# Kernel optimization log

Hardware: AMD Instinct MI355X
Metric: run time of the kernel (lower is better)

Reference implementation:

```python
import jax, jax.numpy as jnp
import numpy as np

ALPHA = 0.2  # LeakyReLU negative slope
NEG_INF = -9e15  # matches torch -9000000000000000.0


def setup_inputs() -> dict:
    key = jax.random.key(0)
    k1, k2, k3, k4, k5, k6 = jax.random.split(key, 6)
    N, F_in, F_out = 4096, 512, 256
    adj = jax.random.randint(k1, (N, N), 0, 2, dtype=jnp.int32)
    h = jax.random.normal(k2, (N, F_in), dtype=jnp.float32)
    # proj: Linear(F_in, F_out)
    W = jax.random.normal(k3, (F_in, F_out), dtype=jnp.float32) * (1.0 / np.sqrt(F_in))
    b = jax.random.normal(k4, (F_out,), dtype=jnp.float32) * 0.01
    # proj_a: Linear(2*F_out, 1) split into the two halves acting on src/dst features
    a1 = jax.random.normal(k5, (F_out,), dtype=jnp.float32) * (1.0 / np.sqrt(2 * F_out))
    a2 = jax.random.normal(k6, (F_out,), dtype=jnp.float32) * (1.0 / np.sqrt(2 * F_out))
    a_b = jnp.zeros((), dtype=jnp.float32)
    return {"adj": adj, "h": h, "W": W, "b": b, "a1": a1, "a2": a2, "a_b": a_b}


def reference(adj, h, W, b, a1, a2, a_b):
    # wh = proj(h): [N, F_out]
    wh = h @ W + b
    # Fused form of the N x N x 2F concat + Linear(2F,1):
    # logits[i, j] = wh[i] . a1 + wh[j] . a2 + a_b
    f_src = wh @ a1  # [N]
    f_dst = wh @ a2  # [N]
    e = jax.nn.leaky_relu(f_src[:, None] + f_dst[None, :] + a_b, negative_slope=ALPHA)
    e = jnp.where(adj > 0, e, NEG_INF)
    att = jax.nn.softmax(e, axis=-1)  # F.softmax legacy dim=1 for 2D
    # dropout: inference mode (no-op) for deterministic reference
    out = att @ wh  # [N, F_out]
    return jax.nn.elu(out)  # concat=True
```

## Files before the change

kernel.cpp:

```cpp
#include <hip/hip_runtime.h>

#define NN   4096
#define FIN  512
#define FOUT 256
#define ALPHA 0.2f

typedef __attribute__((ext_vector_type(8))) short short8;
typedef __attribute__((ext_vector_type(4))) float f32x4;
typedef unsigned short u16;

__device__ __forceinline__ u16 f2bf(float x) {
    union { float f; unsigned u; } v; v.f = x;
    unsigned r = v.u + 0x7FFF + ((v.u >> 16) & 1);
    return (u16)(r >> 16);
}

__global__ __launch_bounds__(256) void k_wt(const float* __restrict__ W,
                                            u16* __restrict__ Wt) {
    __shared__ float s[64 * 65];
    const int t  = threadIdx.x;
    const int f0 = blockIdx.x * 64;
    const int k0 = blockIdx.y * 64;
    #pragma unroll
    for (int p = 0; p < 4; ++p) {
        int q = t + 256 * p, rr = q >> 4, cc = q & 15;
        float4 w4 = *(const float4*)&W[(size_t)(k0 + rr) * FOUT + f0 + cc * 4];
        s[(cc * 4 + 0) * 65 + rr] = w4.x;
        s[(cc * 4 + 1) * 65 + rr] = w4.y;
        s[(cc * 4 + 2) * 65 + rr] = w4.z;
        s[(cc * 4 + 3) * 65 + rr] = w4.w;
    }
    __syncthreads();
    #pragma unroll
    for (int p = 0; p < 4; ++p) {
        int q = t + 256 * p, f = q >> 4, kg = q & 15;
        ushort4 o;
        o.x = f2bf(s[f * 65 + kg * 4 + 0]);
        o.y = f2bf(s[f * 65 + kg * 4 + 1]);
        o.z = f2bf(s[f * 65 + kg * 4 + 2]);
        o.w = f2bf(s[f * 65 + kg * 4 + 3]);
        *(ushort4*)&Wt[(size_t)(f0 + f) * FIN + k0 + kg * 4] = o;
    }
}

#define HS 520
__global__ __launch_bounds__(256) void k_proj(const float* __restrict__ h,
                                              const u16* __restrict__ Wt,
                                              const float* __restrict__ bias,
                                              const float* __restrict__ a1,
                                              const float* __restrict__ a2,
                                              u16* __restrict__ whT,
                                              float* __restrict__ psrc,
                                              float* __restrict__ pdst) {
    __shared__ u16   s_h[32 * HS];
    __shared__ float s_red[4 * 32];
    const int t  = threadIdx.x;
    const int f0 = blockIdx.x * 64;
    const int i0 = blockIdx.y * 32;
    #pragma unroll
    for (int p = 0; p < 16; ++p) {
        int q = t + 256 * p, row = q >> 7, c4 = q & 127;
        float4 v = *(const float4*)&h[(size_t)(i0 + row) * FIN + c4 * 4];
        ushort4 o; o.x = f2bf(v.x); o.y = f2bf(v.y); o.z = f2bf(v.z); o.w = f2bf(v.w);
        *(ushort4*)&s_h[row * HS + c4 * 4] = o;
    }
    __syncthreads();
    const int w = t >> 6, l = t & 63, n = l & 15, quad = l >> 4;
    const int hh = w & 1, fh = w >> 1;
    f32x4 acc[2] = {{0.f,0.f,0.f,0.f},{0.f,0.f,0.f,0.f}};
    #pragma unroll
    for (int k0 = 0; k0 < FIN; k0 += 32) {
        short8 a  = *(const short8*)&s_h[(hh * 16 + n) * HS + k0 + quad * 8];
        short8 b0 = *(const short8*)&Wt[(size_t)(f0 + fh * 32 + n) * FIN + k0 + quad * 8];
        short8 b1 = *(const short8*)&Wt[(size_t)(f0 + fh * 32 + 16 + n) * FIN + k0 + quad * 8];
        acc[0] = __builtin_amdgcn_mfma_f32_16x16x32_bf16(a, b0, acc[0], 0, 0, 0);
        acc[1] = __builtin_amdgcn_mfma_f32_16x16x32_bf16(a, b1, acc[1], 0, 0, 0);
    }
    u16* wt_tile = whT + (size_t)(i0 >> 5) * (FOUT * 32);
    float a1v[2], a2v[2];
    a1v[0] = a1[f0 + fh * 32 + n];      a1v[1] = a1[f0 + fh * 32 + 16 + n];
    a2v[0] = a2[f0 + fh * 32 + n];      a2v[1] = a2[f0 + fh * 32 + 16 + n];
    float ps[4] = {0.f,0.f,0.f,0.f}, pd[4] = {0.f,0.f,0.f,0.f};
    #pragma unroll
    for (int u = 0; u < 2; ++u) {
        const int f = f0 + fh * 32 + u * 16 + n;
        const float bv = bias[f];
        #pragma unroll
        for (int r = 0; r < 4; ++r) {
            float val = acc[u][r] + bv;
            wt_tile[f * 32 + hh * 16 + quad * 4 + r] = f2bf(val);
            ps[r] += val * a1v[u];
            pd[r] += val * a2v[u];
        }
    }
    #pragma unroll
    for (int m = 1; m < 16; m <<= 1) {
        #pragma unroll
        for (int r = 0; r < 4; ++r) { ps[r] += __shfl_xor(ps[r], m); pd[r] += __shfl_xor(pd[r], m); }
    }
    if (n == 0) {
        #pragma unroll
        for (int r = 0; r < 4; ++r) {
            int il = hh * 16 + quad * 4 + r;
            s_red[fh * 32 + il]       = ps[r];
            s_red[64 + fh * 32 + il]  = pd[r];
        }
    }
    __syncthreads();
    if (t < 32) {
        psrc[(size_t)blockIdx.x * NN + i0 + t] = s_red[t]      + s_red[32 + t];
        pdst[(size_t)blockIdx.x * NN + i0 + t] = s_red[64 + t] + s_red[96 + t];
    }
}

#define BI 16
#define TJ 32
#define CC 4
#define JCHUNK (NN / CC)
#define NITER  (JCHUNK / TJ)
__global__ __launch_bounds__(256) void k_attn(const int* __restrict__ adj,
                                              const u16* __restrict__ whT,
                                              const float* __restrict__ psrc,
                                              const float* __restrict__ pdst,
                                              const float* __restrict__ ab,
                                              float* __restrict__ part,
                                              float* __restrict__ psum) {
    __shared__ float s_fd[JCHUNK];
    const int t  = threadIdx.x;
    const int i0 = blockIdx.x * BI;
    const int c  = blockIdx.y;
    const int jbeg = c * JCHUNK;
    const int w = t >> 6, l = t & 63, n = l & 15, quad = l >> 4;

    {
        float4 v0 = ((const float4*)&pdst[jbeg])[t];
        float4 v1 = ((const float4*)&pdst[NN + jbeg])[t];
        float4 v2 = ((const float4*)&pdst[2 * NN + jbeg])[t];
        float4 v3 = ((const float4*)&pdst[3 * NN + jbeg])[t];
        float4 o;
        o.x = v0.x + v1.x + v2.x + v3.x; o.y = v0.y + v1.y + v2.y + v3.y;
        o.z = v0.z + v1.z + v2.z + v3.z; o.w = v0.w + v1.w + v2.w + v3.w;
        ((float4*)s_fd)[t] = o;
    }
    const float fsm = psrc[i0 + n] + psrc[NN + i0 + n] + psrc[2 * NN + i0 + n]
                    + psrc[3 * NN + i0 + n] + ab[0];
    __syncthreads();

    const int* arow = adj + (size_t)(i0 + n) * NN + jbeg + quad * 8;
    int4 a0 = *(const int4*)arow;
    int4 a1 = *(const int4*)(arow + 4);

    f32x4 acc[4] = {{0.f,0.f,0.f,0.f},{0.f,0.f,0.f,0.f},{0.f,0.f,0.f,0.f},{0.f,0.f,0.f,0.f}};
    float rs = 0.f;

    for (int it = 0; it < NITER; ++it) {
        const int jo = it * TJ;
        float4 g0 = *(const float4*)&s_fd[jo + quad * 8];
        float4 g1 = *(const float4*)&s_fd[jo + quad * 8 + 4];
        short8 af;
        {
            float x, p;
            x = fsm + g0.x; x = x > 0.f ? x : ALPHA * x; p = a0.x > 0 ? __expf(x) : 0.f; af[0] = (short)f2bf(p); rs += p;
            x = fsm + g0.y; x = x > 0.f ? x : ALPHA * x; p = a0.y > 0 ? __expf(x) : 0.f; af[1] = (short)f2bf(p); rs += p;
            x = fsm + g0.z; x = x > 0.f ? x : ALPHA * x; p = a0.z > 0 ? __expf(x) : 0.f; af[2] = (short)f2bf(p); rs += p;
            x = fsm + g0.w; x = x > 0.f ? x : ALPHA * x; p = a0.w > 0 ? __expf(x) : 0.f; af[3] = (short)f2bf(p); rs += p;
            x = fsm + g1.x; x = x > 0.f ? x : ALPHA * x; p = a1.x > 0 ? __expf(x) : 0.f; af[4] = (short)f2bf(p); rs += p;
            x = fsm + g1.y; x = x > 0.f ? x : ALPHA * x; p = a1.y > 0 ? __expf(x) : 0.f; af[5] = (short)f2bf(p); rs += p;
            x = fsm + g1.z; x = x > 0.f ? x : ALPHA * x; p = a1.z > 0 ? __expf(x) : 0.f; af[6] = (short)f2bf(p); rs += p;
            x = fsm + g1.w; x = x > 0.f ? x : ALPHA * x; p = a1.w > 0 ? __expf(x) : 0.f; af[7] = (short)f2bf(p); rs += p;
        }
        if (it + 1 < NITER) {
            a0 = *(const int4*)(arow + TJ);
            a1 = *(const int4*)(arow + TJ + 4);
            arow += TJ;
        }
        const u16* tb = whT + (size_t)((jbeg + jo) >> 5) * (FOUT * 32) + quad * 8;
        #pragma unroll
        for (int u = 0; u < 4; ++u) {
            short8 b = *(const short8*)&tb[(w * 64 + u * 16 + n) * 32];
            acc[u] = __builtin_amdgcn_mfma_f32_16x16x32_bf16(af, b, acc[u], 0, 0, 0);
        }
    }
    rs += __shfl_xor(rs, 16);
    rs += __shfl_xor(rs, 32);
    if (t < BI) psum[(size_t)c * NN + i0 + t] = rs;
    float* pc = part + ((size_t)c * NN + i0) * FOUT + w * 64;
    #pragma unroll
    for (int u = 0; u < 4; ++u)
        #pragma unroll
        for (int r = 0; r < 4; ++r)
            pc[(size_t)(quad * 4 + r) * FOUT + u * 16 + n] = acc[u][r];
}

__global__ __launch_bounds__(256) void k_fin(const float* __restrict__ part,
                                             const float* __restrict__ psum,
                                             float* __restrict__ out) {
    const int g = blockIdx.x * 256 + threadIdx.x;
    const int i = g >> 6;
    const size_t s4 = (size_t)NN * (FOUT / 4);
    float4 a = ((const float4*)part)[g];
    float s = psum[i];
    #pragma unroll
    for (int c = 1; c < CC; ++c) {
        float4 bb = ((const float4*)part)[g + (size_t)c * s4];
        a.x += bb.x; a.y += bb.y; a.z += bb.z; a.w += bb.w;
        s += psum[(size_t)c * NN + i];
    }
    const float inv = 1.0f / s;
    a.x *= inv; a.y *= inv; a.z *= inv; a.w *= inv;
    a.x = a.x > 0.f ? a.x : __expf(a.x) - 1.f;
    a.y = a.y > 0.f ? a.y : __expf(a.y) - 1.f;
    a.z = a.z > 0.f ? a.z : __expf(a.z) - 1.f;
    a.w = a.w > 0.f ? a.w : __expf(a.w) - 1.f;
    ((float4*)out)[g] = a;
}

extern "C" void kernel_launch(void* const* d_in, const int* in_sizes, int n_in,
                              void* d_out, int out_size, void* d_ws, size_t ws_size,
                              hipStream_t stream) {
    const int*   adj = (const int*)  d_in[0];
    const float* h   = (const float*)d_in[1];
    const float* W   = (const float*)d_in[2];
    const float* b   = (const float*)d_in[3];
    const float* a1  = (const float*)d_in[4];
    const float* a2  = (const float*)d_in[5];
    const float* ab  = (const float*)d_in[6];
    float* out = (float*)d_out;

    float* psrc = (float*)d_ws;
    float* pdst = psrc + 4 * (size_t)NN;
    float* psum = pdst + 4 * (size_t)NN;
    float* part = psum + (size_t)CC * NN;
    u16*   Wt   = (u16*)(part + (size_t)CC * NN * FOUT);
    u16*   whT  = Wt + (size_t)FOUT * FIN;

    k_wt  <<<dim3(FOUT / 64, FIN / 64), 256, 0, stream>>>(W, Wt);
    k_proj<<<dim3(FOUT / 64, NN / 32), 256, 0, stream>>>(h, Wt, b, a1, a2, whT, psrc, pdst);
    k_attn<<<dim3(NN / BI, CC), 256, 0, stream>>>(adj, whT, psrc, pdst, ab, part, psum);
    k_fin <<<(NN * FOUT / 4) / 256, 256, 0, stream>>>(part, psum, out);
}
```

Baseline: 184.1 us.

## Factor exp out of attention logits and retile attention kernel per-wave rows

Replaces the per-element exp of the leaky-ReLU logit with precomputed exp(fd) and exp(0.2*fd) tables in shared memory. Each element becomes a compare-and-select against exp(-fs) plus a multiply; the dropped exp(fs) row factor cancels in the softmax normalization. Each wave now owns 16 distinct rows and all 256 output columns, with 16 MFMA accumulators instead of 4. The j-dimension split is doubled to 8 chunks and the kernel requests 2 blocks per SM. The trade-offs are more register pressure and twice the partial-sum traffic for the final reduction kernel, plus some overflow and rounding risk in the factored exponentials.

```diff
diff --git a/kernel.cpp b/kernel.cpp
--- a/kernel.cpp
+++ b/kernel.cpp
@@ -113,61 +113,73 @@
     }
 }
 
-#define BI 16
+#define CC 8
+#define JCHUNK (NN / CC)
 #define TJ 32
-#define CC 4
-#define JCHUNK (NN / CC)
 #define NITER  (JCHUNK / TJ)
-__global__ __launch_bounds__(256) void k_attn(const int* __restrict__ adj,
-                                              const u16* __restrict__ whT,
-                                              const float* __restrict__ psrc,
-                                              const float* __restrict__ pdst,
-                                              const float* __restrict__ ab,
-                                              float* __restrict__ part,
-                                              float* __restrict__ psum) {
-    __shared__ float s_fd[JCHUNK];
+__global__ __launch_bounds__(256, 2) void k_attn(const int* __restrict__ adj,
+                                                 const u16* __restrict__ whT,
+                                                 const float* __restrict__ psrc,
+                                                 const float* __restrict__ pdst,
+                                                 const float* __restrict__ ab,
+                                                 float* __restrict__ part,
+                                                 float* __restrict__ psum) {
+    __shared__ float s_F[JCHUNK];
+    __shared__ float s_H[JCHUNK];
     const int t  = threadIdx.x;
-    const int i0 = blockIdx.x * BI;
     const int c  = blockIdx.y;
     const int jbeg = c * JCHUNK;
     const int w = t >> 6, l = t & 63, n = l & 15, quad = l >> 4;
-
-    {
+    const int i0w = blockIdx.x * 64 + w * 16;
+
+    if (t < JCHUNK / 4) {
         float4 v0 = ((const float4*)&pdst[jbeg])[t];
         float4 v1 = ((const float4*)&pdst[NN + jbeg])[t];
         float4 v2 = ((const float4*)&pdst[2 * NN + jbeg])[t];
         float4 v3 = ((const float4*)&pdst[3 * NN + jbeg])[t];
-        float4 o;
-        o.x = v0.x + v1.x + v2.x + v3.x; o.y = v0.y + v1.y + v2.y + v3.y;
-        o.z = v0.z + v1.z + v2.z + v3.z; o.w = v0.w + v1.w + v2.w + v3.w;
-        ((float4*)s_fd)[t] = o;
-    }
-    const float fsm = psrc[i0 + n] + psrc[NN + i0 + n] + psrc[2 * NN + i0 + n]
-                    + psrc[3 * NN + i0 + n] + ab[0];
-    __syncthreads();
-
-    const int* arow = adj + (size_t)(i0 + n) * NN + jbeg + quad * 8;
+        float4 fd4;
+        fd4.x = v0.x + v1.x + v2.x + v3.x; fd4.y = v0.y + v1.y + v2.y + v3.y;
+        fd4.z = v0.z + v1.z + v2.z + v3.z; fd4.w = v0.w + v1.w + v2.w + v3.w;
+        float4 F4, H4;
+        F4.x = __expf(fd4.x); F4.y = __expf(fd4.y); F4.z = __expf(fd4.z); F4.w = __expf(fd4.w);
+        H4.x = __expf(0.2f * fd4.x); H4.y = __expf(0.2f * fd4.y);
+        H4.z = __expf(0.2f * fd4.z); H4.w = __expf(0.2f * fd4.w);
+        ((float4*)s_F)[t] = F4;
+        ((float4*)s_H)[t] = H4;
+    }
+    const float fsm = psrc[i0w + n] + psrc[NN + i0w + n] + psrc[2 * NN + i0w + n]
+                    + psrc[3 * NN + i0w + n] + ab[0];
+    const float Ein = __expf(-fsm);
+    const float Rn  = __expf(-0.8f * fsm);
+    __syncthreads();
+
+    const int* arow = adj + (size_t)(i0w + n) * NN + jbeg + quad * 8;
     int4 a0 = *(const int4*)arow;
     int4 a1 = *(const int4*)(arow + 4);
 
-    f32x4 acc[4] = {{0.f,0.f,0.f,0.f},{0.f,0.f,0.f,0.f},{0.f,0.f,0.f,0.f},{0.f,0.f,0.f,0.f}};
+    f32x4 acc[16];
+    #pragma unroll
+    for (int u = 0; u < 16; ++u) acc[u] = (f32x4){0.f, 0.f, 0.f, 0.f};
     float rs = 0.f;
 
     for (int it = 0; it < NITER; ++it) {
         const int jo = it * TJ;
-        float4 g0 = *(const float4*)&s_fd[jo + quad * 8];
-        float4 g1 = *(const float4*)&s_fd[jo + quad * 8 + 4];
+        float4 F0 = *(const float4*)&s_F[jo + quad * 8];
+        float4 F1 = *(const float4*)&s_F[jo + quad * 8 + 4];
+        float4 H0 = *(const float4*)&s_H[jo + quad * 8];
+        float4 H1 = *(const float4*)&s_H[jo + quad * 8 + 4];
         short8 af;
         {
-            float x, p;
-            x = fsm + g0.x; x = x > 0.f ? x : ALPHA * x; p = a0.x > 0 ? __expf(x) : 0.f; af[0] = (short)f2bf(p); rs += p;
-            x = fsm + g0.y; x = x > 0.f ? x : ALPHA * x; p = a0.y > 0 ? __expf(x) : 0.f; af[1] = (short)f2bf(p); rs += p;
-            x = fsm + g0.z; x = x > 0.f ? x : ALPHA * x; p = a0.z > 0 ? __expf(x) : 0.f; af[2] = (short)f2bf(p); rs += p;
-            x = fsm + g0.w; x = x > 0.f ? x : ALPHA * x; p = a0.w > 0 ? __expf(x) : 0.f; af[3] = (short)f2bf(p); rs += p;
-            x = fsm + g1.x; x = x > 0.f ? x : ALPHA * x; p = a1.x > 0 ? __expf(x) : 0.f; af[4] = (short)f2bf(p); rs += p;
-            x = fsm + g1.y; x = x > 0.f ? x : ALPHA * x; p = a1.y > 0 ? __expf(x) : 0.f; af[5] = (short)f2bf(p); rs += p;
-            x = fsm + g1.z; x = x > 0.f ? x : ALPHA * x; p = a1.z > 0 ? __expf(x) : 0.f; af[6] = (short)f2bf(p); rs += p;
-            x = fsm + g1.w; x = x > 0.f ? x : ALPHA * x; p = a1.w > 0 ? __expf(x) : 0.f; af[7] = (short)f2bf(p); rs += p;
+            float qq;
+#define MK(e, Fc, Hc, Ac) \
+            qq = (Fc > Ein) ? Fc : Rn * Hc; \
+            qq = (Ac > 0) ? qq : 0.f; \
+            af[e] = (short)f2bf(qq); rs += qq;
+            MK(0, F0.x, H0.x, a0.x)  MK(1, F0.y, H0.y, a0.y)
+            MK(2, F0.z, H0.z, a0.z)  MK(3, F0.w, H0.w, a0.w)
+            MK(4, F1.x, H1.x, a1.x)  MK(5, F1.y, H1.y, a1.y)
+            MK(6, F1.z, H1.z, a1.z)  MK(7, F1.w, H1.w, a1.w)
+#undef MK
         }
         if (it + 1 < NITER) {
             a0 = *(const int4*)(arow + TJ);
@@ -176,17 +188,17 @@
         }
         const u16* tb = whT + (size_t)((jbeg + jo) >> 5) * (FOUT * 32) + quad * 8;
         #pragma unroll
-        for (int u = 0; u < 4; ++u) {
-            short8 b = *(const short8*)&tb[(w * 64 + u * 16 + n) * 32];
+        for (int u = 0; u < 16; ++u) {
+            short8 b = *(const short8*)&tb[(u * 16 + n) * 32];
             acc[u] = __builtin_amdgcn_mfma_f32_16x16x32_bf16(af, b, acc[u], 0, 0, 0);
         }
     }
     rs += __shfl_xor(rs, 16);
     rs += __shfl_xor(rs, 32);
-    if (t < BI) psum[(size_t)c * NN + i0 + t] = rs;
-    float* pc = part + ((size_t)c * NN + i0) * FOUT + w * 64;
-    #pragma unroll
-    for (int u = 0; u < 4; ++u)
+    if (l < 16) psum[(size_t)c * NN + i0w + l] = rs;
+    float* pc = part + ((size_t)c * NN + i0w) * FOUT;
+    #pragma unroll
+    for (int u = 0; u < 16; ++u)
         #pragma unroll
         for (int r = 0; r < 4; ++r)
             pc[(size_t)(quad * 4 + r) * FOUT + u * 16 + n] = acc[u][r];
@@ -236,6 +248,6 @@
 
     k_wt  <<<dim3(FOUT / 64, FIN / 64), 256, 0, stream>>>(W, Wt);
     k_proj<<<dim3(FOUT / 64, NN / 32), 256, 0, stream>>>(h, Wt, b, a1, a2, whT, psrc, pdst);
-    k_attn<<<dim3(NN / BI, CC), 256, 0, stream>>>(adj, whT, psrc, pdst, ab, part, psum);
+    k_attn<<<dim3(NN / 64, CC), 256, 0, stream>>>(adj, whT, psrc, pdst, ab, part, psum);
     k_fin <<<(NN * FOUT / 4) / 256, 256, 0, stream>>>(part, psum, out);
 }
```

Measured after the change: 178.6 us. -3.0%, faster.
